# Optimization experiments

Measured on AMD Instinct MI355X. Metric: run time of the kernel, lower is better.

Reference implementation:

```python
import jax, jax.numpy as jnp
import numpy as np

N = 4096   # num_nodes
D_E = 16   # node embedding dim
H = 4      # heads
K = 3      # Chebyshev order
L = 64     # in_dim
B = 16     # batch


def setup_inputs() -> dict:
    key = jax.random.key(0)
    ks = jax.random.split(key, 8)
    return {
        "x": jax.random.normal(ks[0], (B, N, L), dtype=jnp.float32),
        "psi_emb": jax.random.normal(ks[1], (N, D_E), dtype=jnp.float32),
        "psi": jnp.asarray(1.0, dtype=jnp.float32),
        "W_q": jax.random.normal(ks[2], (D_E, H, D_E), dtype=jnp.float32),
        "W_k": jax.random.normal(ks[3], (D_E, H, D_E), dtype=jnp.float32),
        "attn_alpha": jnp.asarray(0.5, dtype=jnp.float32),
        "F_w": jax.random.normal(ks[4], (H, D_E, K + 1, L), dtype=jnp.float32),
        "f_b": jax.random.normal(ks[5], (H, D_E), dtype=jnp.float32),
        "head_mix": jnp.ones((H,), dtype=jnp.float32),
    }


def reference(x, psi_emb, psi, W_q, W_k, attn_alpha, F_w, f_b, head_mix):
    # x: (B, N, L) -> out: (B, N)
    Bx, Nx, Lx = x.shape

    # Gaussian adjacency: softmax over rows of exp(-psi * ||psi_i - psi_j||^2)
    diff = psi_emb[:, None, :] - psi_emb[None, :, :]      # (N, N, d_e)
    dist2 = jnp.sum(diff * diff, axis=-1)                 # (N, N)
    A_g = jax.nn.softmax(jnp.exp(-psi * dist2), axis=1)   # (N, N)

    # Per-head attention adjacency
    Q = jnp.einsum('nd,dhm->nhm', psi_emb, W_q)           # (N, H, d_e)
    Kt = jnp.einsum('nd,dhm->nhm', psi_emb, W_k)          # (N, H, d_e)
    scale = 1.0 / np.sqrt(Q.shape[-1]).astype(np.float32)
    attn = jnp.einsum('nhd,mhd->hnm', Q, Kt) * scale      # (H, N, N)
    A_attn = jax.nn.softmax(attn, axis=-1)

    # Sigmoid blend of gaussian and attention adjacencies
    alpha = jax.nn.sigmoid(attn_alpha)
    A_effs = alpha * A_g[None, :, :] + (1.0 - alpha) * A_attn  # (H, N, N)

    mix_w = jax.nn.softmax(head_mix)                      # (H,)
    I = jnp.eye(Nx, dtype=x.dtype)

    out = jnp.zeros((Bx, Nx), dtype=x.dtype)
    for h in range(H):  # small fixed head loop (structurally distinct params)
        A = A_effs[h]
        # Chebyshev recursion: T0=I, T1=A, Tk = 2 A T_{k-1} - T_{k-2}
        supports = [I, A]
        for _ in range(2, K + 1):
            supports.append(2.0 * (A @ supports[-1]) - supports[-2])
        S = jnp.stack(supports, axis=0)                   # (K+1, N, N)

        # Per-node filter weights / bias from node embeddings
        W_filter = jnp.einsum('nd,dkl->nkl', psi_emb, F_w[h])  # (N, K+1, L)
        b_filter = psi_emb @ f_b[h]                            # (N,)

        x_g = jnp.einsum('knm,bml->bknl', S, x)                # (B, K+1, N, L)
        out_h = jnp.einsum('bknl,nkl->bn', x_g, W_filter) + b_filter
        out = out + mix_w[h] * out_h
    return out
```

## Files before the change

kernel.cpp:

```cpp
#include <hip/hip_runtime.h>
#include <hip/hip_bf16.h>

#define NN 4096
#define DE 16
#define NH 4
#define LL 64
#define NB 16
#define CC 1024

typedef __attribute__((ext_vector_type(8))) short short8v;
typedef __attribute__((ext_vector_type(4))) float f32x4;

#define GLD_LDS16(gp, lp) __builtin_amdgcn_global_load_lds( \
    (const __attribute__((address_space(1))) unsigned int*)(gp), \
    (__attribute__((address_space(3))) unsigned int*)(lp), 16, 0, 0)

__device__ __forceinline__ unsigned short f2bf(float f){
  unsigned int u = __float_as_uint(f);
  u += 0x7fffu + ((u >> 16) & 1u);
  return (unsigned short)(u >> 16);
}
__device__ __forceinline__ float bf2f(unsigned short s){
  return __uint_as_float(((unsigned int)s) << 16);
}
__device__ __forceinline__ void get_mix(const float* hm, float* mw){
  float a=hm[0],b=hm[1],c=hm[2],d=hm[3];
  float m = fmaxf(fmaxf(a,b),fmaxf(c,d));
  float e0=__expf(a-m),e1=__expf(b-m),e2=__expf(c-m),e3=__expf(d-m);
  float inv = 1.0f/(e0+e1+e2+e3);
  mw[0]=e0*inv; mw[1]=e1*inv; mw[2]=e2*inv; mw[3]=e3*inv;
}

__global__ void k_prep(const float* __restrict__ psi_emb, const float* __restrict__ W_q,
                       const float* __restrict__ W_k, const float* __restrict__ f_b,
                       const float* __restrict__ head_mix,
                       unsigned short* __restrict__ Qh, unsigned short* __restrict__ Ql,
                       unsigned short* __restrict__ Kh, unsigned short* __restrict__ Kl,
                       unsigned short* __restrict__ Ph, unsigned short* __restrict__ Pl,
                       float* __restrict__ n2g, float* __restrict__ bias_comb){
  int n = blockIdx.x*blockDim.x + threadIdx.x;
  if (n >= NN) return;
  float p[DE];
  float n2 = 0.f;
  unsigned short ph[DE], pl[DE];
  #pragma unroll
  for (int d=0;d<DE;d++){
    p[d] = psi_emb[n*DE+d];
    n2 += p[d]*p[d];
    ph[d] = f2bf(p[d]);
    pl[d] = f2bf(p[d] - bf2f(ph[d]));
  }
  n2g[n] = n2;
  *(short8v*)(Ph + n*DE)     = *(short8v*)ph;
  *(short8v*)(Ph + n*DE + 8) = *(short8v*)(ph+8);
  *(short8v*)(Pl + n*DE)     = *(short8v*)pl;
  *(short8v*)(Pl + n*DE + 8) = *(short8v*)(pl+8);
  float mw[NH]; get_mix(head_mix, mw);
  float bias = 0.f;
  for (int h=0; h<NH; h++){
    unsigned short qh[DE], ql[DE], kh[DE], kl[DE];
    #pragma unroll
    for (int m=0;m<DE;m++){
      float q=0.f,k=0.f;
      #pragma unroll
      for (int d=0;d<DE;d++){
        q += p[d]*W_q[(d*NH+h)*DE+m];
        k += p[d]*W_k[(d*NH+h)*DE+m];
      }
      qh[m]=f2bf(q); ql[m]=f2bf(q - bf2f(qh[m]));
      kh[m]=f2bf(k); kl[m]=f2bf(k - bf2f(kh[m]));
    }
    size_t base = ((size_t)h*NN + n)*DE;
    *(short8v*)(Qh+base)=*(short8v*)qh;   *(short8v*)(Qh+base+8)=*(short8v*)(qh+8);
    *(short8v*)(Ql+base)=*(short8v*)ql;   *(short8v*)(Ql+base+8)=*(short8v*)(ql+8);
    *(short8v*)(Kh+base)=*(short8v*)kh;   *(short8v*)(Kh+base+8)=*(short8v*)(kh+8);
    *(short8v*)(Kl+base)=*(short8v*)kl;   *(short8v*)(Kl+base+8)=*(short8v*)(kl+8);
    float bh=0.f;
    #pragma unroll
    for (int d=0;d<DE;d++) bh += p[d]*f_b[h*DE+d];
    bias += mw[h]*bh;
  }
  bias_comb[n]=bias;
}

__global__ void k_wf(const float* __restrict__ psi_emb, const float* __restrict__ F_w,
                     const float* __restrict__ head_mix,
                     float* __restrict__ Wf_eff, float* __restrict__ W0c){
  int id = blockIdx.x*256 + threadIdx.x;
  int n = id & (NN-1);
  int kl = id >> 12;
  int l = kl & (LL-1);
  int k = kl >> 6;
  float mw[NH]; get_mix(head_mix, mw);
  float p[DE];
  #pragma unroll
  for (int d=0;d<DE;d++) p[d]=psi_emb[n*DE+d];
  float s0=0.f;
  for (int h=0;h<NH;h++){
    float v=0.f;
    #pragma unroll
    for (int d=0;d<DE;d++) v += p[d]*F_w[((h*DE+d)*4+k)*LL+l];
    v *= mw[h];
    Wf_eff[(((size_t)(h*4+k))*LL+l)*NN+n]=v;
    s0 += v;
  }
  if (k==0) W0c[(size_t)l*NN+n]=s0;
}

__global__ __launch_bounds__(256, 4) void k_adj(
    const unsigned short* __restrict__ Qh, const unsigned short* __restrict__ Ql,
    const unsigned short* __restrict__ Kh, const unsigned short* __restrict__ Kl,
    const unsigned short* __restrict__ Ph, const unsigned short* __restrict__ Pl,
    const float* __restrict__ n2g, const float* __restrict__ psi_p,
    const float* __restrict__ attn_alpha, unsigned short* __restrict__ A_all){
  __shared__ unsigned short T[4][16][72];
  __shared__ float st_g[4][16], st_m[4][16], st_s[4][16];
  __shared__ float fin_g[16], fin_m[16], fin_s[16];

  int tid = threadIdx.x;
  int lane = tid & 63, w = tid >> 6;
  int h = blockIdx.y;
  int n0 = blockIdx.x * 16;
  int kg = lane >> 4;
  int cl = lane & 15;
  float psi_v = psi_p[0];
  float alpha = 1.f/(1.f+__expf(-attn_alpha[0]));

  short8v z8 = {};
  int rown = n0 + cl;
  const unsigned short* qb = ((kg<2) ? Qh : Ql) + ((size_t)h*NN + rown)*DE + (kg&1)*8;
  const unsigned short* pb = ((kg<2) ? Ph : Pl) + (size_t)rown*DE + (kg&1)*8;
  short8v aF1 = *(const short8v*)qb;
  short8v gA1 = *(const short8v*)pb;
  short8v aF2 = z8, gA2 = z8;
  if (kg < 2){ aF2 = aF1; gA2 = gA1; }

  float n2row[4];
  #pragma unroll
  for (int r=0;r<4;r++) n2row[r] = n2g[n0 + kg*4 + r];

  float gsum[4], mx[4], sm[4];
  #pragma unroll
  for (int r=0;r<4;r++){ gsum[r]=0.f; mx[r]=-1e30f; sm[r]=0.f; }

  const size_t hN = (size_t)h*NN;
  int mbase = w * 1024;

  #pragma unroll 2
  for (int mt=0; mt<64; ++mt){
    int m0 = mbase + mt*16;
    int mm = m0 + cl;
    const unsigned short* kb = Kh + (hN + mm)*DE + (kg&1)*8;
    const unsigned short* pmb = Ph + (size_t)mm*DE + (kg&1)*8;
    short8v bF1 = *(const short8v*)kb;
    short8v gB1 = *(const short8v*)pmb;
    short8v bF2 = z8, gB2 = z8;
    if (kg < 2){
      bF2 = *(const short8v*)(Kl + (hN + mm)*DE + (kg&1)*8);
      gB2 = *(const short8v*)(Pl + (size_t)mm*DE + (kg&1)*8);
    }
    f32x4 zc = {};
    f32x4 sc = __builtin_amdgcn_mfma_f32_16x16x32_bf16(aF2, bF2, zc, 0,0,0);
    sc = __builtin_amdgcn_mfma_f32_16x16x32_bf16(aF1, bF1, sc, 0,0,0);
    f32x4 gc = __builtin_amdgcn_mfma_f32_16x16x32_bf16(gA2, gB2, zc, 0,0,0);
    gc = __builtin_amdgcn_mfma_f32_16x16x32_bf16(gA1, gB1, gc, 0,0,0);
    float n2m = n2g[m0 + cl];
    #pragma unroll
    for (int r=0;r<4;r++){
      float s = sc[r]*0.25f;
      float d2 = n2row[r] + n2m - 2.f*gc[r];
      float eg = __expf(__expf(-psi_v*d2));
      gsum[r] += eg;
      if (s > mx[r] + 8.f){
        sm[r] = sm[r]*__expf(mx[r]-s) + 1.f;
        mx[r] = s;
      } else {
        sm[r] += __expf(s - mx[r]);
      }
    }
  }
  #pragma unroll
  for (int off=1; off<16; off<<=1){
    #pragma unroll
    for (int r=0;r<4;r++){
      gsum[r] += __shfl_xor(gsum[r], off);
      float om = __shfl_xor(mx[r], off);
      float os = __shfl_xor(sm[r], off);
      float nm = fmaxf(mx[r], om);
      sm[r] = sm[r]*__expf(mx[r]-nm) + os*__expf(om-nm);
      mx[r] = nm;
    }
  }
  if (cl < 4){
    float g,m,s;
    if      (cl==0){ g=gsum[0]; m=mx[0]; s=sm[0]; }
    else if (cl==1){ g=gsum[1]; m=mx[1]; s=sm[1]; }
    else if (cl==2){ g=gsum[2]; m=mx[2]; s=sm[2]; }
    else           { g=gsum[3]; m=mx[3]; s=sm[3]; }
    int row = kg*4 + cl;
    st_g[w][row]=g; st_m[w][row]=m; st_s[w][row]=s;
  }
  __syncthreads();
  if (tid < 16){
    float G=0.f, M=-1e30f, S=0.f;
    #pragma unroll
    for (int ww=0; ww<4; ww++){
      G += st_g[ww][tid];
      float om = st_m[ww][tid], os = st_s[ww][tid];
      float nm = fmaxf(M, om);
      S = S*__expf(M-nm) + os*__expf(om-nm);
      M = nm;
    }
    fin_g[tid] = 1.f/G;
    fin_m[tid] = M;
    fin_s[tid] = 1.f/S;
  }
  __syncthreads();

  float fg[4], fm[4], fs[4];
  #pragma unroll
  for (int r=0;r<4;r++){
    fg[r]=fin_g[kg*4+r]; fm[r]=fin_m[kg*4+r]; fs[r]=fin_s[kg*4+r];
  }
  float a1 = alpha, a2 = 1.f - alpha;

  for (int mt=0; mt<64; ++mt){
    int m0 = mbase + mt*16;
    int mm = m0 + cl;
    const unsigned short* kb = Kh + (hN + mm)*DE + (kg&1)*8;
    const unsigned short* pmb = Ph + (size_t)mm*DE + (kg&1)*8;
    short8v bF1 = *(const short8v*)kb;
    short8v gB1 = *(const short8v*)pmb;
    short8v bF2 = z8, gB2 = z8;
    if (kg < 2){
      bF2 = *(const short8v*)(Kl + (hN + mm)*DE + (kg&1)*8);
      gB2 = *(const short8v*)(Pl + (size_t)mm*DE + (kg&1)*8);
    }
    f32x4 zc = {};
    f32x4 sc = __builtin_amdgcn_mfma_f32_16x16x32_bf16(aF2, bF2, zc, 0,0,0);
    sc = __builtin_amdgcn_mfma_f32_16x16x32_bf16(aF1, bF1, sc, 0,0,0);
    f32x4 gc = __builtin_amdgcn_mfma_f32_16x16x32_bf16(gA2, gB2, zc, 0,0,0);
    gc = __builtin_amdgcn_mfma_f32_16x16x32_bf16(gA1, gB1, gc, 0,0,0);
    float n2m = n2g[m0 + cl];
    #pragma unroll
    for (int r=0;r<4;r++){
      float s = sc[r]*0.25f;
      float d2 = n2row[r] + n2m - 2.f*gc[r];
      float eg = __expf(__expf(-psi_v*d2));
      float ag  = eg * fg[r];
      float aat = __expf(s - fm[r]) * fs[r];
      float a = a1*ag + a2*aat;
      T[w][kg*4+r][(mt&3)*16 + cl] = f2bf(a);
    }
    if ((mt & 3) == 3){
      int row = lane >> 2, cgp = lane & 3;
      short8v v0 = *(const short8v*)&T[w][row][cgp*16];
      short8v v1 = *(const short8v*)&T[w][row][cgp*16+8];
      unsigned short* dst = A_all + hN*NN + (size_t)(n0+row)*NN + mbase + (mt&~3)*16 + cgp*16;
      *(short8v*)dst = v0;
      *(short8v*)(dst+8) = v1;
    }
  }
}

__global__ __launch_bounds__(256) void k_xpose(const float* __restrict__ x,
                                               unsigned short* __restrict__ X){
  __shared__ float t[64][65];
  int b = blockIdx.y, n0 = blockIdx.x*64;
  int tid=threadIdx.x;
  int nr = tid>>2, lc=(tid&3)*16;
  const float* src = x + ((size_t)b*NN + n0 + nr)*LL + lc;
  #pragma unroll
  for (int j=0;j<16;j+=4){
    float4 v = *(const float4*)(src + j);
    t[nr][lc+j+0]=v.x; t[nr][lc+j+1]=v.y; t[nr][lc+j+2]=v.z; t[nr][lc+j+3]=v.w;
  }
  __syncthreads();
  int cl = tid>>2, mp=(tid&3)*16;
  short8v bufv[2];
  #pragma unroll
  for (int j=0;j<16;j++) bufv[j>>3][j&7] = (short)f2bf(t[mp+j][cl]);
  unsigned short* dst = X + (size_t)(b*LL+cl)*NN + n0 + mp;
  *(short8v*)dst = bufv[0];
  *(short8v*)(dst+8) = bufv[1];
}

__global__ void k_out0(const float* __restrict__ x, const float* __restrict__ W0c,
                       const float* __restrict__ bias_comb, float* __restrict__ out){
  int id = blockIdx.x*256+threadIdx.x;
  int n = id & (NN-1);
  float acc = bias_comb[n];
  const float* xp = x + (size_t)id*LL;
  #pragma unroll
  for (int l4=0;l4<LL;l4+=4){
    float4 xv = *(const float4*)(xp+l4);
    acc += xv.x*W0c[(size_t)(l4+0)*NN+n] + xv.y*W0c[(size_t)(l4+1)*NN+n]
         + xv.z*W0c[(size_t)(l4+2)*NN+n] + xv.w*W0c[(size_t)(l4+3)*NN+n];
  }
  out[id] = acc;
}

template<int HAS_PREV, int STORE>
__global__ __launch_bounds__(256) void k_cheb(
    const unsigned short* __restrict__ A_all,
    const unsigned short* __restrict__ Zin, size_t z_hs,
    const unsigned short* __restrict__ Yprev, size_t p_hs,
    unsigned short* __restrict__ Ynew, size_t y_hs,
    const float* __restrict__ Wf_eff, float* __restrict__ out,
    int kcheb, float scale)
{
  __shared__ __align__(16) unsigned short ZT[2][128][64];
  __shared__ __align__(16) unsigned short AT[2][128][64];
  int h = blockIdx.z;
  int n0 = blockIdx.x * 128;
  int c0 = blockIdx.y * 128;
  const unsigned short* Ah = A_all + (size_t)h*NN*NN;
  const unsigned short* Z  = Zin + z_hs*h;
  int tid = threadIdx.x;
  int lane = tid & 63, w = tid >> 6;
  int wr = w >> 1, wc = w & 1;
  f32x4 acc[4][4] = {};

  int lrow8 = lane >> 3;
  int scol  = ((lane & 7) ^ lrow8) * 8;
  const unsigned short* gA = Ah + (size_t)(n0 + w*32 + lrow8)*NN + scol;
  const unsigned short* gZ = Z  + (size_t)(c0 + w*32 + lrow8)*NN + scol;

  int frow = lane & 15;
  int rsw  = frow & 7;
  int fsl  = lane >> 4;
  int s0 = ((0 + fsl) ^ rsw) * 8;
  int s1 = ((4 + fsl) ^ rsw) * 8;
  const unsigned short* zs0 = &ZT[0][wr*64 + frow][0] + s0;
  const unsigned short* zs1 = &ZT[0][wr*64 + frow][0] + s1;
  const unsigned short* as0 = &AT[0][wc*64 + frow][0] + s0;
  const unsigned short* as1 = &AT[0][wc*64 + frow][0] + s1;

#define STAGE(B, MO) do { \
    _Pragma("unroll") \
    for (int jj = 0; jj < 4; ++jj) { \
      GLD_LDS16(gA + (size_t)(8*jj)*NN + (MO), &AT[B][w*32 + 8*jj][0]); \
      GLD_LDS16(gZ + (size_t)(8*jj)*NN + (MO), &ZT[B][w*32 + 8*jj][0]); \
    } \
  } while(0)

#define COMPUTE(B) do { \
    short8v af0[4], af1[4], bf0[4], bf1[4]; \
    _Pragma("unroll") \
    for (int i=0;i<4;i++){ \
      af0[i] = *(const short8v*)(zs0 + (B)*8192 + i*1024); \
      af1[i] = *(const short8v*)(zs1 + (B)*8192 + i*1024); \
      bf0[i] = *(const short8v*)(as0 + (B)*8192 + i*1024); \
      bf1[i] = *(const short8v*)(as1 + (B)*8192 + i*1024); \
    } \
    _Pragma("unroll") \
    for (int i=0;i<4;i++) \
      _Pragma("unroll") \
      for (int j=0;j<4;j++) \
        acc[i][j] = __builtin_amdgcn_mfma_f32_16x16x32_bf16(af0[i], bf0[j], acc[i][j], 0,0,0); \
    _Pragma("unroll") \
    for (int i=0;i<4;i++) \
      _Pragma("unroll") \
      for (int j=0;j<4;j++) \
        acc[i][j] = __builtin_amdgcn_mfma_f32_16x16x32_bf16(af1[i], bf1[j], acc[i][j], 0,0,0); \
  } while(0)

#define BARRIER() do { __builtin_amdgcn_s_barrier(); __builtin_amdgcn_sched_barrier(0); } while(0)

  STAGE(0, 0);
  int mo = 64;
  for (int tp = 0; tp < 31; ++tp) {
    BARRIER();
    STAGE(1, mo); mo += 64;
    asm volatile("s_waitcnt vmcnt(8)" ::: "memory");
    BARRIER();
    COMPUTE(0);
    BARRIER();
    STAGE(0, mo); mo += 64;
    asm volatile("s_waitcnt vmcnt(8)" ::: "memory");
    BARRIER();
    COMPUTE(1);
  }
  BARRIER();
  STAGE(1, mo);
  asm volatile("s_waitcnt vmcnt(8)" ::: "memory");
  BARRIER();
  COMPUTE(0);
  BARRIER();
  asm volatile("s_waitcnt vmcnt(0)" ::: "memory");
  BARRIER();
  COMPUTE(1);

#undef STAGE
#undef COMPUTE
#undef BARRIER

  int b = (c0 >> 6) + wr;
  int g4 = lane >> 4, nl = lane & 15;
  #pragma unroll
  for (int j=0;j<4;j++){
    int n = n0 + wc*64 + j*16 + nl;
    float psum = 0.f;
    #pragma unroll
    for (int i=0;i<4;i++){
      #pragma unroll
      for (int r=0;r<4;r++){
        int lx = i*16 + 4*g4 + r;
        size_t cn = (size_t)(b*64 + lx)*NN + n;
        float v = scale*acc[i][j][r];
        if (HAS_PREV) v -= bf2f(Yprev[p_hs*h + cn]);
        if (STORE) Ynew[y_hs*h + cn] = f2bf(v);
        psum += v * Wf_eff[(((size_t)(h*4 + kcheb))*LL + lx)*NN + n];
      }
    }
    psum += __shfl_xor(psum, 16);
    psum += __shfl_xor(psum, 32);
    if (g4 == 0) atomicAdd(out + (size_t)b*NN + n, psum);
  }
}

extern "C" void kernel_launch(void* const* d_in, const int* in_sizes, int n_in,
                              void* d_out, int out_size, void* d_ws, size_t ws_size,
                              hipStream_t stream) {
  const float* x         = (const float*)d_in[0];
  const float* psi_emb   = (const float*)d_in[1];
  const float* psi       = (const float*)d_in[2];
  const float* W_q       = (const float*)d_in[3];
  const float* W_k       = (const float*)d_in[4];
  const float* attn_alpha= (const float*)d_in[5];
  const float* F_w       = (const float*)d_in[6];
  const float* f_b       = (const float*)d_in[7];
  const float* head_mix  = (const float*)d_in[8];
  float* out = (float*)d_out;

  char* ws = (char*)d_ws;
  size_t off = 0;
  auto alloc = [&](size_t bytes)->void*{
    void* p = ws + off; off += (bytes + 255) & ~(size_t)255; return p;
  };
  unsigned short* A_all  = (unsigned short*)alloc((size_t)NH*NN*NN*2);
  unsigned short* X      = (unsigned short*)alloc((size_t)CC*NN*2);
  unsigned short* Y1     = (unsigned short*)alloc((size_t)NH*CC*NN*2);
  unsigned short* Y2     = (unsigned short*)alloc((size_t)NH*CC*NN*2);
  float* Wf_eff  = (float*)alloc((size_t)NH*4*LL*NN*4);
  float* W0c     = (float*)alloc((size_t)LL*NN*4);
  unsigned short* Qh = (unsigned short*)alloc((size_t)NH*NN*DE*2);
  unsigned short* Ql = (unsigned short*)alloc((size_t)NH*NN*DE*2);
  unsigned short* Kh = (unsigned short*)alloc((size_t)NH*NN*DE*2);
  unsigned short* Kl = (unsigned short*)alloc((size_t)NH*NN*DE*2);
  unsigned short* Ph = (unsigned short*)alloc((size_t)NN*DE*2);
  unsigned short* Pl = (unsigned short*)alloc((size_t)NN*DE*2);
  float* n2g     = (float*)alloc((size_t)NN*4);
  float* bias_c  = (float*)alloc((size_t)NN*4);

  k_prep<<<dim3(16), dim3(256), 0, stream>>>(psi_emb, W_q, W_k, f_b, head_mix,
                                             Qh, Ql, Kh, Kl, Ph, Pl, n2g, bias_c);
  k_wf<<<dim3(4096), dim3(256), 0, stream>>>(psi_emb, F_w, head_mix, Wf_eff, W0c);
  k_adj<<<dim3(256, NH), dim3(256), 0, stream>>>(Qh, Ql, Kh, Kl, Ph, Pl, n2g,
                                                 psi, attn_alpha, A_all);
  k_xpose<<<dim3(64, NB), dim3(256), 0, stream>>>(x, X);
  k_out0<<<dim3(256), dim3(256), 0, stream>>>(x, W0c, bias_c, out);

  dim3 gg(32, 8, NH);
  size_t CN = (size_t)CC*NN;
  k_cheb<0,1><<<gg, dim3(256), 0, stream>>>(A_all, X, (size_t)0, X, (size_t)0,
                                            Y1, CN, Wf_eff, out, 1, 1.0f);
  k_cheb<1,1><<<gg, dim3(256), 0, stream>>>(A_all, Y1, CN, X, (size_t)0,
                                            Y2, CN, Wf_eff, out, 2, 2.0f);
  k_cheb<1,0><<<gg, dim3(256), 0, stream>>>(A_all, Y2, CN, Y1, CN,
                                            Y2, (size_t)0, Wf_eff, out, 3, 2.0f);
  (void)in_sizes; (void)n_in; (void)out_size; (void)ws_size;
}
```

Before: 666.0 us.

## Fuse all heads into one adjacency block to share Gaussian computation

The adjacency kernel now handles all four heads inside one 512-thread block per 16-row tile instead of a separate block per head. The Gaussian kernel term (two MFMAs plus a double exp) is computed once and reused across heads, where before it was recomputed four times. In exchange the grid shrinks to 256 blocks with launch bounds (512,1), and per-head softmax state held in registers raises register pressure, which can lower occupancy and latency hiding.

```diff
diff --git a/kernel.cpp b/kernel.cpp
--- a/kernel.cpp
+++ b/kernel.cpp
@@ -107,156 +107,176 @@
   if (k==0) W0c[(size_t)l*NN+n]=s0;
 }
 
-__global__ __launch_bounds__(256, 4) void k_adj(
+__global__ __launch_bounds__(512, 1) void k_adj(
     const unsigned short* __restrict__ Qh, const unsigned short* __restrict__ Ql,
     const unsigned short* __restrict__ Kh, const unsigned short* __restrict__ Kl,
     const unsigned short* __restrict__ Ph, const unsigned short* __restrict__ Pl,
     const float* __restrict__ n2g, const float* __restrict__ psi_p,
     const float* __restrict__ attn_alpha, unsigned short* __restrict__ A_all){
-  __shared__ unsigned short T[4][16][72];
-  __shared__ float st_g[4][16], st_m[4][16], st_s[4][16];
-  __shared__ float fin_g[16], fin_m[16], fin_s[16];
+  __shared__ float st_g[8][16];
+  __shared__ float st_m[8][NH][16], st_s[8][NH][16];
+  __shared__ float fin_g[16];
+  __shared__ float fin_m[NH][16], fin_s[NH][16];
+  __shared__ unsigned short T[8][16][72];
 
   int tid = threadIdx.x;
   int lane = tid & 63, w = tid >> 6;
-  int h = blockIdx.y;
   int n0 = blockIdx.x * 16;
-  int kg = lane >> 4;
-  int cl = lane & 15;
+  int kg = lane >> 4, cl = lane & 15;
   float psi_v = psi_p[0];
   float alpha = 1.f/(1.f+__expf(-attn_alpha[0]));
 
   short8v z8 = {};
   int rown = n0 + cl;
-  const unsigned short* qb = ((kg<2) ? Qh : Ql) + ((size_t)h*NN + rown)*DE + (kg&1)*8;
-  const unsigned short* pb = ((kg<2) ? Ph : Pl) + (size_t)rown*DE + (kg&1)*8;
-  short8v aF1 = *(const short8v*)qb;
-  short8v gA1 = *(const short8v*)pb;
-  short8v aF2 = z8, gA2 = z8;
-  if (kg < 2){ aF2 = aF1; gA2 = gA1; }
+  short8v gA1 = *(const short8v*)(((kg<2)?Ph:Pl) + (size_t)rown*DE + (kg&1)*8);
+  short8v aF[NH];
+  #pragma unroll
+  for (int h=0;h<NH;h++)
+    aF[h] = *(const short8v*)(((kg<2)?Qh:Ql) + ((size_t)h*NN+rown)*DE + (kg&1)*8);
 
   float n2row[4];
   #pragma unroll
   for (int r=0;r<4;r++) n2row[r] = n2g[n0 + kg*4 + r];
 
-  float gsum[4], mx[4], sm[4];
-  #pragma unroll
-  for (int r=0;r<4;r++){ gsum[r]=0.f; mx[r]=-1e30f; sm[r]=0.f; }
-
-  const size_t hN = (size_t)h*NN;
-  int mbase = w * 1024;
-
-  #pragma unroll 2
-  for (int mt=0; mt<64; ++mt){
-    int m0 = mbase + mt*16;
-    int mm = m0 + cl;
-    const unsigned short* kb = Kh + (hN + mm)*DE + (kg&1)*8;
-    const unsigned short* pmb = Ph + (size_t)mm*DE + (kg&1)*8;
-    short8v bF1 = *(const short8v*)kb;
-    short8v gB1 = *(const short8v*)pmb;
-    short8v bF2 = z8, gB2 = z8;
-    if (kg < 2){
-      bF2 = *(const short8v*)(Kl + (hN + mm)*DE + (kg&1)*8);
-      gB2 = *(const short8v*)(Pl + (size_t)mm*DE + (kg&1)*8);
-    }
+  float gsum[4];
+  float mx[NH][4], sm[NH][4];
+  #pragma unroll
+  for (int r=0;r<4;r++) gsum[r]=0.f;
+  #pragma unroll
+  for (int h=0;h<NH;h++)
+    #pragma unroll
+    for (int r=0;r<4;r++){ mx[h][r]=-1e30f; sm[h][r]=0.f; }
+
+  int mbase = w * 512;
+
+  for (int mt=0; mt<32; ++mt){
+    int mm = mbase + mt*16 + cl;
+    short8v gB1 = *(const short8v*)(Ph + (size_t)mm*DE + (kg&1)*8);
+    short8v gB2 = (kg<2) ? *(const short8v*)(Pl + (size_t)mm*DE + (kg&1)*8) : z8;
     f32x4 zc = {};
-    f32x4 sc = __builtin_amdgcn_mfma_f32_16x16x32_bf16(aF2, bF2, zc, 0,0,0);
-    sc = __builtin_amdgcn_mfma_f32_16x16x32_bf16(aF1, bF1, sc, 0,0,0);
-    f32x4 gc = __builtin_amdgcn_mfma_f32_16x16x32_bf16(gA2, gB2, zc, 0,0,0);
+    f32x4 gc = __builtin_amdgcn_mfma_f32_16x16x32_bf16(gA1, gB2, zc, 0,0,0);
     gc = __builtin_amdgcn_mfma_f32_16x16x32_bf16(gA1, gB1, gc, 0,0,0);
-    float n2m = n2g[m0 + cl];
+    float n2m = n2g[mm];
     #pragma unroll
     for (int r=0;r<4;r++){
-      float s = sc[r]*0.25f;
       float d2 = n2row[r] + n2m - 2.f*gc[r];
-      float eg = __expf(__expf(-psi_v*d2));
-      gsum[r] += eg;
-      if (s > mx[r] + 8.f){
-        sm[r] = sm[r]*__expf(mx[r]-s) + 1.f;
-        mx[r] = s;
-      } else {
-        sm[r] += __expf(s - mx[r]);
+      gsum[r] += __expf(__expf(-psi_v*d2));
+    }
+    #pragma unroll
+    for (int h=0;h<NH;h++){
+      size_t hb = ((size_t)h*NN + mm)*DE + (kg&1)*8;
+      short8v bF1 = *(const short8v*)(Kh + hb);
+      short8v bF2 = (kg<2) ? *(const short8v*)(Kl + hb) : z8;
+      f32x4 sc = __builtin_amdgcn_mfma_f32_16x16x32_bf16(aF[h], bF2, zc, 0,0,0);
+      sc = __builtin_amdgcn_mfma_f32_16x16x32_bf16(aF[h], bF1, sc, 0,0,0);
+      #pragma unroll
+      for (int r=0;r<4;r++){
+        float s = sc[r]*0.25f;
+        if (s > mx[h][r] + 8.f){
+          sm[h][r] = sm[h][r]*__expf(mx[h][r]-s) + 1.f;
+          mx[h][r] = s;
+        } else {
+          sm[h][r] += __expf(s - mx[h][r]);
+        }
       }
     }
   }
   #pragma unroll
   for (int off=1; off<16; off<<=1){
     #pragma unroll
-    for (int r=0;r<4;r++){
-      gsum[r] += __shfl_xor(gsum[r], off);
-      float om = __shfl_xor(mx[r], off);
-      float os = __shfl_xor(sm[r], off);
-      float nm = fmaxf(mx[r], om);
-      sm[r] = sm[r]*__expf(mx[r]-nm) + os*__expf(om-nm);
-      mx[r] = nm;
-    }
+    for (int r=0;r<4;r++) gsum[r] += __shfl_xor(gsum[r], off);
+    #pragma unroll
+    for (int h=0;h<NH;h++)
+      #pragma unroll
+      for (int r=0;r<4;r++){
+        float om = __shfl_xor(mx[h][r], off);
+        float os = __shfl_xor(sm[h][r], off);
+        float nm = fmaxf(mx[h][r], om);
+        sm[h][r] = sm[h][r]*__expf(mx[h][r]-nm) + os*__expf(om-nm);
+        mx[h][r] = nm;
+      }
   }
   if (cl < 4){
-    float g,m,s;
-    if      (cl==0){ g=gsum[0]; m=mx[0]; s=sm[0]; }
-    else if (cl==1){ g=gsum[1]; m=mx[1]; s=sm[1]; }
-    else if (cl==2){ g=gsum[2]; m=mx[2]; s=sm[2]; }
-    else           { g=gsum[3]; m=mx[3]; s=sm[3]; }
-    int row = kg*4 + cl;
-    st_g[w][row]=g; st_m[w][row]=m; st_s[w][row]=s;
+    #pragma unroll
+    for (int rr=0; rr<4; rr++) if (cl == rr){
+      st_g[w][kg*4+rr] = gsum[rr];
+      #pragma unroll
+      for (int h=0;h<NH;h++){
+        st_m[w][h][kg*4+rr] = mx[h][rr];
+        st_s[w][h][kg*4+rr] = sm[h][rr];
+      }
+    }
   }
   __syncthreads();
-  if (tid < 16){
-    float G=0.f, M=-1e30f, S=0.f;
-    #pragma unroll
-    for (int ww=0; ww<4; ww++){
-      G += st_g[ww][tid];
-      float om = st_m[ww][tid], os = st_s[ww][tid];
+  if (tid < 64){
+    int h = tid >> 4, row = tid & 15;
+    float M=-1e30f, S=0.f, G=0.f;
+    #pragma unroll
+    for (int ww=0; ww<8; ww++){
+      if (h==0) G += st_g[ww][row];
+      float om = st_m[ww][h][row], os = st_s[ww][h][row];
       float nm = fmaxf(M, om);
       S = S*__expf(M-nm) + os*__expf(om-nm);
       M = nm;
     }
-    fin_g[tid] = 1.f/G;
-    fin_m[tid] = M;
-    fin_s[tid] = 1.f/S;
+    fin_m[h][row] = M;
+    fin_s[h][row] = 1.f/S;
+    if (h==0) fin_g[row] = 1.f/G;
   }
   __syncthreads();
 
-  float fg[4], fm[4], fs[4];
-  #pragma unroll
-  for (int r=0;r<4;r++){
-    fg[r]=fin_g[kg*4+r]; fm[r]=fin_m[kg*4+r]; fs[r]=fin_s[kg*4+r];
-  }
+  float fg[4], fm[NH][4], fs[NH][4];
+  #pragma unroll
+  for (int r=0;r<4;r++) fg[r] = fin_g[kg*4+r];
+  #pragma unroll
+  for (int h=0;h<NH;h++)
+    #pragma unroll
+    for (int r=0;r<4;r++){
+      fm[h][r] = fin_m[h][kg*4+r];
+      fs[h][r] = fin_s[h][kg*4+r];
+    }
   float a1 = alpha, a2 = 1.f - alpha;
 
-  for (int mt=0; mt<64; ++mt){
-    int m0 = mbase + mt*16;
-    int mm = m0 + cl;
-    const unsigned short* kb = Kh + (hN + mm)*DE + (kg&1)*8;
-    const unsigned short* pmb = Ph + (size_t)mm*DE + (kg&1)*8;
-    short8v bF1 = *(const short8v*)kb;
-    short8v gB1 = *(const short8v*)pmb;
-    short8v bF2 = z8, gB2 = z8;
-    if (kg < 2){
-      bF2 = *(const short8v*)(Kl + (hN + mm)*DE + (kg&1)*8);
-      gB2 = *(const short8v*)(Pl + (size_t)mm*DE + (kg&1)*8);
-    }
-    f32x4 zc = {};
-    f32x4 sc = __builtin_amdgcn_mfma_f32_16x16x32_bf16(aF2, bF2, zc, 0,0,0);
-    sc = __builtin_amdgcn_mfma_f32_16x16x32_bf16(aF1, bF1, sc, 0,0,0);
-    f32x4 gc = __builtin_amdgcn_mfma_f32_16x16x32_bf16(gA2, gB2, zc, 0,0,0);
-    gc = __builtin_amdgcn_mfma_f32_16x16x32_bf16(gA1, gB1, gc, 0,0,0);
-    float n2m = n2g[m0 + cl];
-    #pragma unroll
-    for (int r=0;r<4;r++){
-      float s = sc[r]*0.25f;
-      float d2 = n2row[r] + n2m - 2.f*gc[r];
-      float eg = __expf(__expf(-psi_v*d2));
-      float ag  = eg * fg[r];
-      float aat = __expf(s - fm[r]) * fs[r];
-      float a = a1*ag + a2*aat;
-      T[w][kg*4+r][(mt&3)*16 + cl] = f2bf(a);
-    }
-    if ((mt & 3) == 3){
-      int row = lane >> 2, cgp = lane & 3;
-      short8v v0 = *(const short8v*)&T[w][row][cgp*16];
-      short8v v1 = *(const short8v*)&T[w][row][cgp*16+8];
-      unsigned short* dst = A_all + hN*NN + (size_t)(n0+row)*NN + mbase + (mt&~3)*16 + cgp*16;
+  for (int mtg=0; mtg<8; ++mtg){
+    float ag[4][4];
+    #pragma unroll
+    for (int mtl=0; mtl<4; ++mtl){
+      int mm = mbase + (mtg*4+mtl)*16 + cl;
+      short8v gB1 = *(const short8v*)(Ph + (size_t)mm*DE + (kg&1)*8);
+      short8v gB2 = (kg<2) ? *(const short8v*)(Pl + (size_t)mm*DE + (kg&1)*8) : z8;
+      f32x4 zc = {};
+      f32x4 gc = __builtin_amdgcn_mfma_f32_16x16x32_bf16(gA1, gB2, zc, 0,0,0);
+      gc = __builtin_amdgcn_mfma_f32_16x16x32_bf16(gA1, gB1, gc, 0,0,0);
+      float n2m = n2g[mm];
+      #pragma unroll
+      for (int r=0;r<4;r++){
+        float d2 = n2row[r] + n2m - 2.f*gc[r];
+        ag[mtl][r] = __expf(__expf(-psi_v*d2)) * fg[r];
+      }
+    }
+    #pragma unroll
+    for (int h=0;h<NH;h++){
+      #pragma unroll
+      for (int mtl=0; mtl<4; ++mtl){
+        int mm = mbase + (mtg*4+mtl)*16 + cl;
+        size_t hb = ((size_t)h*NN + mm)*DE + (kg&1)*8;
+        short8v bF1 = *(const short8v*)(Kh + hb);
+        short8v bF2 = (kg<2) ? *(const short8v*)(Kl + hb) : z8;
+        f32x4 zc = {};
+        f32x4 sc = __builtin_amdgcn_mfma_f32_16x16x32_bf16(aF[h], bF2, zc, 0,0,0);
+        sc = __builtin_amdgcn_mfma_f32_16x16x32_bf16(aF[h], bF1, sc, 0,0,0);
+        #pragma unroll
+        for (int r=0;r<4;r++){
+          float aat = __expf(sc[r]*0.25f - fm[h][r]) * fs[h][r];
+          float a = a1*ag[mtl][r] + a2*aat;
+          T[w][kg*4+r][mtl*16 + cl] = f2bf(a);
+        }
+      }
+      int rowX = lane >> 2, cgp = lane & 3;
+      short8v v0 = *(const short8v*)&T[w][rowX][cgp*16];
+      short8v v1 = *(const short8v*)&T[w][rowX][cgp*16+8];
+      unsigned short* dst = A_all + (size_t)h*NN*NN + (size_t)(n0+rowX)*NN
+                          + mbase + mtg*64 + cgp*16;
       *(short8v*)dst = v0;
       *(short8v*)(dst+8) = v1;
     }
@@ -456,8 +476,8 @@
   k_prep<<<dim3(16), dim3(256), 0, stream>>>(psi_emb, W_q, W_k, f_b, head_mix,
                                              Qh, Ql, Kh, Kl, Ph, Pl, n2g, bias_c);
   k_wf<<<dim3(4096), dim3(256), 0, stream>>>(psi_emb, F_w, head_mix, Wf_eff, W0c);
-  k_adj<<<dim3(256, NH), dim3(256), 0, stream>>>(Qh, Ql, Kh, Kl, Ph, Pl, n2g,
-                                                 psi, attn_alpha, A_all);
+  k_adj<<<dim3(256), dim3(512), 0, stream>>>(Qh, Ql, Kh, Kl, Ph, Pl, n2g,
+                                             psi, attn_alpha, A_all);
   k_xpose<<<dim3(64, NB), dim3(256), 0, stream>>>(x, X);
   k_out0<<<dim3(256), dim3(256), 0, stream>>>(x, W0c, bias_c, out);
 
```

Result: slower. 692.6 us (+4.0%).
